# Optimization experiments

Measured on AMD Instinct MI355X. Metric: run time of the kernel, lower is better.

The kernel has to match this reference:

```python
import jax, jax.numpy as jnp
import numpy as np

Q, G, H, K, C, O = 20000, 20000, 32, 15, 128, 128


def setup_inputs() -> dict:
    key = jax.random.key(0)
    k1, k2, k3, k4, k5, k6 = jax.random.split(key, 6)
    return {
        "query_points": jax.random.normal(k1, (Q, 3), dtype=jnp.float32),
        "support_points": jax.random.normal(k2, (G, 3), dtype=jnp.float32),
        "support_features": jax.random.normal(k3, (G, C), dtype=jnp.float32),
        "kernel": jax.random.normal(k4, (K, 3), dtype=jnp.float32),
        "weights": jax.random.normal(k5, (K, C, O), dtype=jnp.float32),
        # KDTree KNN indices are precomputed int constants; random in-range
        # indices give identical math/perf characteristics.
        "neighbor_indices": jax.random.randint(k6, (Q, H), 0, G, dtype=jnp.int32),
    }


def reference(query_points, support_points, support_features, kernel, weights, neighbor_indices):
    # Faithful to original: neighbor_points gathered from query_points
    # (original code indexes query_points, not support_points; requires Q == G).
    neighbor_points = query_points[neighbor_indices]          # [Q, H, 3]
    neighbor_features = support_features[neighbor_indices]    # [Q, H, C]
    # diff: [Q, H, K, 3] = neighbor - query - kernel_point
    diff = neighbor_points[:, :, None, :] - query_points[:, None, None, :] - kernel
    distances = jnp.sqrt(jnp.sum(diff * diff, axis=-1))        # [Q, H, K]
    sigma = 1.0
    influences = jax.nn.relu(1.0 - distances / sigma)          # [Q, H, K]
    # 3-way contraction over h, k, c  -> [Q, O]
    result = jnp.einsum("qhk,kco,qhc->qo", influences, weights, neighbor_features)
    return result
```

## Files before the change

### kernel.cpp

```cpp
#include <hip/hip_runtime.h>


typedef short bf16x8 __attribute__((ext_vector_type(8)));
typedef float f32x4 __attribute__((ext_vector_type(4)));

constexpr int Qn = 20000;
constexpr int Hn = 32;
constexpr int Kn = 15;
constexpr int Cn = 128;
constexpr int On = 128;
constexpr int QB = 16;
constexpr int CK = 2048;
constexpr int KT = CK / 32;
constexpr int NT = On / 16;
constexpr int BLOCK = 512;

constexpr int F_OFF     = 0;
constexpr int NPT_OFF   = 0;
constexpr int DENSE_OFF = 8192;
constexpr int INFL_OFF  = 65536;
constexpr int GLIST_OFF = 81920;
constexpr int NIDX_OFF  = 83968;
constexpr int HLIST_OFF = 86016;
constexpr int CNT_OFF   = 87040;
constexpr int QPL_OFF   = 87104;
constexpr int KPL_OFF   = 87360;
constexpr int FLG_OFF   = 87616;
constexpr int POOL_SZ   = 87680;

__device__ __forceinline__ unsigned short f2bf(float x) {
  unsigned u = __float_as_uint(x);
  unsigned r = u + 0x7fffu + ((u >> 16) & 1u);
  return (unsigned short)(r >> 16);
}

__global__ void conv_w(const float* __restrict__ wts, unsigned short* __restrict__ wfrag) {
  int tid = blockIdx.x * 256 + threadIdx.x;
  if (tid >= KT * NT * 64) return;
  int l = tid & 63, nt = (tid >> 6) & 7, kt = tid >> 9;
  int col = nt * 16 + (l & 15);
  int ck0 = kt * 32 + (l >> 4) * 8;
  unsigned short v[8];
#pragma unroll
  for (int j = 0; j < 8; ++j) {
    int ck = ck0 + j;
    int k = ck & 15, c = ck >> 4;
    v[j] = (k < Kn) ? f2bf(wts[(k * Cn + c) * On + col]) : (unsigned short)0;
  }
  uint4 o;
  o.x = (unsigned)v[0] | ((unsigned)v[1] << 16);
  o.y = (unsigned)v[2] | ((unsigned)v[3] << 16);
  o.z = (unsigned)v[4] | ((unsigned)v[5] << 16);
  o.w = (unsigned)v[6] | ((unsigned)v[7] << 16);
  *(uint4*)(wfrag + (size_t)tid * 8) = o;
}

__global__ __launch_bounds__(BLOCK, 1)
void kpconv_main(const float* __restrict__ qpts,
                 const float* __restrict__ sfeat,
                 const float* __restrict__ kpts,
                 const int* __restrict__ nidx,
                 const unsigned short* __restrict__ wfrag,
                 float* __restrict__ out) {
  __shared__ __align__(16) char pool[POOL_SZ];
  const int t = threadIdx.x;
  const int qbase = blockIdx.x * QB;
  const int l = t & 63, w = t >> 6;
  const int lg = l >> 4, li = l & 15;

  {
    int g = nidx[(size_t)qbase * Hn + t];
    *(int*)(pool + NIDX_OFF + t * 4) = g;
    float* np = (float*)(pool + NPT_OFF + t * 16);
    np[0] = qpts[g * 3 + 0];
    np[1] = qpts[g * 3 + 1];
    np[2] = qpts[g * 3 + 2];
    uint4 z = {0, 0, 0, 0};
    *(uint4*)(pool + INFL_OFF + t * 32) = z;
    *(uint4*)(pool + INFL_OFF + t * 32 + 16) = z;
    if (t < 16) {
      *(unsigned*)(pool + FLG_OFF + t * 4) = 0u;
      float* qp = (float*)(pool + QPL_OFF + t * 16);
      qp[0] = qpts[(qbase + t) * 3 + 0];
      qp[1] = qpts[(qbase + t) * 3 + 1];
      qp[2] = qpts[(qbase + t) * 3 + 2];
    }
    if (t >= 32 && t < 32 + Kn) {
      int k = t - 32;
      float* kp = (float*)(pool + KPL_OFF + k * 16);
      kp[0] = kpts[k * 3 + 0];
      kp[1] = kpts[k * 3 + 1];
      kp[2] = kpts[k * 3 + 2];
    }
  }
  __syncthreads();

#pragma unroll
  for (int it = 0; it < 16; ++it) {
    int idx = t + it * BLOCK;
    int k = idx & 15, h = (idx >> 4) & 31, q = idx >> 9;
    unsigned short v = 0;
    if (k < Kn) {
      const float* np = (const float*)(pool + NPT_OFF + (q * 32 + h) * 16);
      const float* qp = (const float*)(pool + QPL_OFF + q * 16);
      const float* kp = (const float*)(pool + KPL_OFF + k * 16);
      float dx = np[0] - qp[0] - kp[0];
      float dy = np[1] - qp[1] - kp[1];
      float dz = np[2] - qp[2] - kp[2];
      float d = sqrtf(dx * dx + dy * dy + dz * dz);
      float inf = fmaxf(0.f, 1.f - d);
      if (inf > 0.f) atomicOr((unsigned*)(pool + FLG_OFF) + q, 1u << h);
      v = f2bf(inf);
    }
    *(unsigned short*)(pool + DENSE_OFF + q * 1024 + h * 32 + k * 2) = v;
  }
  __syncthreads();

  if (t < 16) {
    unsigned m = *(unsigned*)(pool + FLG_OFF + t * 4);
    int cnt = __popc(m);
    *(int*)(pool + CNT_OFF + t * 4) = cnt;
    int i = 0;
    while (m) {
      int h = __ffs(m) - 1; m &= m - 1;
      *(short*)(pool + HLIST_OFF + t * 64 + i * 2) = (short)h;
      *(int*)(pool + GLIST_OFF + t * 128 + i * 4) = *(int*)(pool + NIDX_OFF + (t * 32 + h) * 4);
      ++i;
    }
  }
  __syncthreads();

#pragma unroll
  for (int it = 0; it < 16; ++it) {
    int idx = t + it * BLOCK;
    int slot = idx & 31, k = (idx >> 5) & 15, q = idx >> 9;
    int cnt = *(const int*)(pool + CNT_OFF + q * 4);
    if (k < Kn && slot < cnt) {
      int h = *(const short*)(pool + HLIST_OFF + q * 64 + slot * 2);
      unsigned short v = *(const unsigned short*)(pool + DENSE_OFF + q * 1024 + h * 32 + k * 2);
      unsigned byte = (unsigned)(q * 1024) + (((unsigned)(k * 64 + slot * 2)) ^ (((unsigned)k & 7u) << 4));
      *(unsigned short*)(pool + INFL_OFF + byte) = v;
    }
  }
  __syncthreads();

  {
    const unsigned abase0 = (unsigned)INFL_OFF +
        (((unsigned)(li * 64 + lg * 16)) ^ (((unsigned)li & 7u) << 4));
    const int cbase = w * 16 + li;
    for (int q = 0; q < QB; ++q) {
      bf16x8 afrag = *(const bf16x8*)(pool + abase0 + q * 1024);
      uint4 ga = *(const uint4*)(pool + GLIST_OFF + q * 128 + lg * 32);
      uint4 gb = *(const uint4*)(pool + GLIST_OFF + q * 128 + lg * 32 + 16);
      int cnt = *(const int*)(pool + CNT_OFF + q * 4);
      int s0 = lg * 8;
      float v0 = (s0 + 0 < cnt) ? sfeat[(size_t)ga.x * Cn + cbase] : 0.f;
      float v1 = (s0 + 1 < cnt) ? sfeat[(size_t)ga.y * Cn + cbase] : 0.f;
      float v2 = (s0 + 2 < cnt) ? sfeat[(size_t)ga.z * Cn + cbase] : 0.f;
      float v3 = (s0 + 3 < cnt) ? sfeat[(size_t)ga.w * Cn + cbase] : 0.f;
      float v4 = (s0 + 4 < cnt) ? sfeat[(size_t)gb.x * Cn + cbase] : 0.f;
      float v5 = (s0 + 5 < cnt) ? sfeat[(size_t)gb.y * Cn + cbase] : 0.f;
      float v6 = (s0 + 6 < cnt) ? sfeat[(size_t)gb.z * Cn + cbase] : 0.f;
      float v7 = (s0 + 7 < cnt) ? sfeat[(size_t)gb.w * Cn + cbase] : 0.f;
      uint4 bu;
      bu.x = (unsigned)f2bf(v0) | ((unsigned)f2bf(v1) << 16);
      bu.y = (unsigned)f2bf(v2) | ((unsigned)f2bf(v3) << 16);
      bu.z = (unsigned)f2bf(v4) | ((unsigned)f2bf(v5) << 16);
      bu.w = (unsigned)f2bf(v6) | ((unsigned)f2bf(v7) << 16);
      bf16x8 bfrag = *(bf16x8*)&bu;
      f32x4 zero = {0.f, 0.f, 0.f, 0.f};
      f32x4 d = __builtin_amdgcn_mfma_f32_16x16x32_bf16(afrag, bfrag, zero, 0, 0, 0);
      unsigned wb = ((unsigned)(cbase * 32 + lg * 8) ^ (((unsigned)q & 7u) << 4)) + (unsigned)(q * 4096);
      uint2 pk;
      pk.x = (unsigned)f2bf(d[0]) | ((unsigned)f2bf(d[1]) << 16);
      pk.y = (unsigned)f2bf(d[2]) | ((unsigned)f2bf(d[3]) << 16);
      *(uint2*)(pool + F_OFF + wb) = pk;
    }
  }
  __syncthreads();

  {
    const int nt = w;
    const unsigned fb = (unsigned)(li * 4096 + lg * 16);
    const unsigned fswz = ((unsigned)li & 7u) << 4;
    const uint4* wf = (const uint4*)wfrag + (size_t)nt * 64 + l;
    f32x4 acc0 = {0.f, 0.f, 0.f, 0.f}, acc1 = {0.f, 0.f, 0.f, 0.f};
#pragma unroll 8
    for (int kt = 0; kt < KT; kt += 2) {
      bf16x8 a0 = *(const bf16x8*)(pool + F_OFF + ((fb + (unsigned)(kt * 64)) ^ fswz));
      uint4 w0 = wf[(size_t)kt * 512];
      bf16x8 a1 = *(const bf16x8*)(pool + F_OFF + ((fb + (unsigned)(kt * 64 + 64)) ^ fswz));
      uint4 w1 = wf[(size_t)kt * 512 + 512];
      acc0 = __builtin_amdgcn_mfma_f32_16x16x32_bf16(a0, *(bf16x8*)&w0, acc0, 0, 0, 0);
      acc1 = __builtin_amdgcn_mfma_f32_16x16x32_bf16(a1, *(bf16x8*)&w1, acc1, 0, 0, 0);
    }
    f32x4 acc = acc0 + acc1;
    float* obase = out + (size_t)qbase * On;
#pragma unroll
    for (int r = 0; r < 4; ++r)
      obase[(lg * 4 + r) * On + nt * 16 + li] = acc[r];
  }
}

extern "C" void kernel_launch(void* const* d_in, const int* in_sizes, int n_in,
                              void* d_out, int out_size, void* d_ws, size_t ws_size,
                              hipStream_t stream) {
  const float* qpts  = (const float*)d_in[0];
  const float* sfeat = (const float*)d_in[2];
  const float* kpts  = (const float*)d_in[3];
  const float* wts   = (const float*)d_in[4];
  const int*   nidx  = (const int*)d_in[5];
  float* outp = (float*)d_out;
  unsigned short* wfrag = (unsigned short*)d_ws;

  conv_w<<<(KT * NT * 64 + 255) / 256, 256, 0, stream>>>(wts, wfrag);
  kpconv_main<<<Qn / QB, BLOCK, 0, stream>>>(qpts, sfeat, kpts, nidx, wfrag, outp);
}
```

Baseline: 190.3 us.

## Split channel contraction into two LDS-halved passes to raise occupancy

```diff
diff --git a/kernel.cpp b/kernel.cpp
--- a/kernel.cpp
+++ b/kernel.cpp
@@ -1,4 +1,5 @@
 #include <hip/hip_runtime.h>
+#include <hip/hip_bf16.h>
 
 
 typedef short bf16x8 __attribute__((ext_vector_type(8)));
@@ -10,57 +11,53 @@
 constexpr int Cn = 128;
 constexpr int On = 128;
 constexpr int QB = 16;
-constexpr int CK = 2048;
-constexpr int KT = CK / 32;
-constexpr int NT = On / 16;
 constexpr int BLOCK = 512;
 
 constexpr int F_OFF     = 0;
 constexpr int NPT_OFF   = 0;
 constexpr int DENSE_OFF = 8192;
-constexpr int INFL_OFF  = 65536;
-constexpr int GLIST_OFF = 81920;
-constexpr int NIDX_OFF  = 83968;
-constexpr int HLIST_OFF = 86016;
-constexpr int CNT_OFF   = 87040;
-constexpr int QPL_OFF   = 87104;
-constexpr int KPL_OFF   = 87360;
-constexpr int FLG_OFF   = 87616;
-constexpr int POOL_SZ   = 87680;
-
-__device__ __forceinline__ unsigned short f2bf(float x) {
-  unsigned u = __float_as_uint(x);
-  unsigned r = u + 0x7fffu + ((u >> 16) & 1u);
-  return (unsigned short)(r >> 16);
-}
-
-__global__ void conv_w(const float* __restrict__ wts, unsigned short* __restrict__ wfrag) {
+constexpr int NIDX_OFF  = 24576;
+constexpr int HLIST_OFF = 26624;
+constexpr int QPL_OFF   = 27648;
+constexpr int KPL_OFF   = 27904;
+constexpr int FLG_OFF   = 28160;
+constexpr int INFL_OFF  = 32768;
+constexpr int GLIST_OFF = 49152;
+constexpr int CNT_OFF   = 51200;
+constexpr int POOL_SZ   = 51264;
+
+__device__ __forceinline__ unsigned short bfu(float x) {
+  union { __hip_bfloat16 h; unsigned short s; } cv;
+  cv.h = __float2bfloat16(x);
+  return cv.s;
+}
+__device__ __forceinline__ unsigned pk2(float a, float b) {
+  union { __hip_bfloat162 h2; unsigned u; } cv;
+  cv.h2 = __float22bfloat162_rn(make_float2(a, b));
+  return cv.u;
+}
+
+__global__ void conv_w(const float* __restrict__ wts, unsigned* __restrict__ wfrag) {
   int tid = blockIdx.x * 256 + threadIdx.x;
-  if (tid >= KT * NT * 64) return;
-  int l = tid & 63, nt = (tid >> 6) & 7, kt = tid >> 9;
-  int col = nt * 16 + (l & 15);
-  int ck0 = kt * 32 + (l >> 4) * 8;
-  unsigned short v[8];
-#pragma unroll
-  for (int j = 0; j < 8; ++j) {
-    int ck = ck0 + j;
-    int k = ck & 15, c = ck >> 4;
-    v[j] = (k < Kn) ? f2bf(wts[(k * Cn + c) * On + col]) : (unsigned short)0;
-  }
-  uint4 o;
-  o.x = (unsigned)v[0] | ((unsigned)v[1] << 16);
-  o.y = (unsigned)v[2] | ((unsigned)v[3] << 16);
-  o.z = (unsigned)v[4] | ((unsigned)v[5] << 16);
-  o.w = (unsigned)v[6] | ((unsigned)v[7] << 16);
-  *(uint4*)(wfrag + (size_t)tid * 8) = o;
-}
-
-__global__ __launch_bounds__(BLOCK, 1)
+  int wsel = tid & 3;
+  int l    = (tid >> 2) & 63;
+  int kt   = (tid >> 8) & 63;
+  int nt   = tid >> 14;
+  int col  = nt * 16 + (l & 15);
+  int ck   = kt * 32 + (l >> 4) * 8 + wsel * 2;
+  int k0 = ck & 15, c0 = ck >> 4;
+  int k1 = k0 + 1;
+  float a = wts[(k0 * Cn + c0) * On + col];
+  float b = (k1 < Kn) ? wts[(k1 * Cn + c0) * On + col] : 0.f;
+  wfrag[tid] = pk2(a, b);
+}
+
+__global__ __launch_bounds__(BLOCK, 4)
 void kpconv_main(const float* __restrict__ qpts,
                  const float* __restrict__ sfeat,
                  const float* __restrict__ kpts,
                  const int* __restrict__ nidx,
-                 const unsigned short* __restrict__ wfrag,
+                 const unsigned* __restrict__ wfrag,
                  float* __restrict__ out) {
   __shared__ __align__(16) char pool[POOL_SZ];
   const int t = threadIdx.x;
@@ -69,15 +66,13 @@
   const int lg = l >> 4, li = l & 15;
 
   {
+    *(unsigned*)(pool + GLIST_OFF + t * 4) = 0u;
     int g = nidx[(size_t)qbase * Hn + t];
     *(int*)(pool + NIDX_OFF + t * 4) = g;
     float* np = (float*)(pool + NPT_OFF + t * 16);
     np[0] = qpts[g * 3 + 0];
     np[1] = qpts[g * 3 + 1];
     np[2] = qpts[g * 3 + 2];
-    uint4 z = {0, 0, 0, 0};
-    *(uint4*)(pool + INFL_OFF + t * 32) = z;
-    *(uint4*)(pool + INFL_OFF + t * 32 + 16) = z;
     if (t < 16) {
       *(unsigned*)(pool + FLG_OFF + t * 4) = 0u;
       float* qp = (float*)(pool + QPL_OFF + t * 16);
@@ -110,7 +105,7 @@
       float d = sqrtf(dx * dx + dy * dy + dz * dz);
       float inf = fmaxf(0.f, 1.f - d);
       if (inf > 0.f) atomicOr((unsigned*)(pool + FLG_OFF) + q, 1u << h);
-      v = f2bf(inf);
+      v = bfu(inf);
     }
     *(unsigned short*)(pool + DENSE_OFF + q * 1024 + h * 32 + k * 2) = v;
   }
@@ -118,13 +113,13 @@
 
   if (t < 16) {
     unsigned m = *(unsigned*)(pool + FLG_OFF + t * 4);
-    int cnt = __popc(m);
-    *(int*)(pool + CNT_OFF + t * 4) = cnt;
+    *(int*)(pool + CNT_OFF + t * 4) = __popc(m);
     int i = 0;
     while (m) {
       int h = __ffs(m) - 1; m &= m - 1;
       *(short*)(pool + HLIST_OFF + t * 64 + i * 2) = (short)h;
-      *(int*)(pool + GLIST_OFF + t * 128 + i * 4) = *(int*)(pool + NIDX_OFF + (t * 32 + h) * 4);
+      *(int*)(pool + GLIST_OFF + t * 128 + i * 4) =
+          *(const int*)(pool + NIDX_OFF + (t * 32 + h) * 4);
       ++i;
     }
   }
@@ -135,24 +130,40 @@
     int idx = t + it * BLOCK;
     int slot = idx & 31, k = (idx >> 5) & 15, q = idx >> 9;
     int cnt = *(const int*)(pool + CNT_OFF + q * 4);
+    unsigned short v = 0;
     if (k < Kn && slot < cnt) {
       int h = *(const short*)(pool + HLIST_OFF + q * 64 + slot * 2);
-      unsigned short v = *(const unsigned short*)(pool + DENSE_OFF + q * 1024 + h * 32 + k * 2);
-      unsigned byte = (unsigned)(q * 1024) + (((unsigned)(k * 64 + slot * 2)) ^ (((unsigned)k & 7u) << 4));
-      *(unsigned short*)(pool + INFL_OFF + byte) = v;
-    }
-  }
-  __syncthreads();
-
-  {
-    const unsigned abase0 = (unsigned)INFL_OFF +
-        (((unsigned)(li * 64 + lg * 16)) ^ (((unsigned)li & 7u) << 4));
-    const int cbase = w * 16 + li;
-    for (int q = 0; q < QB; ++q) {
+      v = *(const unsigned short*)(pool + DENSE_OFF + q * 1024 + h * 32 + k * 2);
+    }
+    unsigned byte = (unsigned)(q * 1024) +
+        (((unsigned)(k * 64 + slot * 2)) ^ (((unsigned)k & 7u) << 4));
+    *(unsigned short*)(pool + INFL_OFF + byte) = v;
+  }
+  __syncthreads();
+
+  const int ctl = w & 3, qg = w >> 2;
+  const unsigned abase0 = (unsigned)INFL_OFF +
+      (((unsigned)(li * 64 + lg * 16)) ^ (((unsigned)li & 7u) << 4));
+  const int cl = ctl * 16 + li;
+  const unsigned wswz = ((unsigned)cl & 7u) << 4;
+  const unsigned wbase0 = (unsigned)((cl >> 1) * 1024 +
+                                     ((cl & 1) * 2 + (lg >> 1)) * 256 +
+                                     (lg & 1) * 8);
+  const unsigned liB = (unsigned)(lg * 256 + li * 16);
+  const unsigned sLg = ((unsigned)(lg >> 1)) << 4;
+  const uint4* wfp = (const uint4*)wfrag + (size_t)w * 4096 + l;
+  f32x4 acc0 = {0.f, 0.f, 0.f, 0.f}, acc1 = {0.f, 0.f, 0.f, 0.f};
+
+#pragma unroll 1
+  for (int r = 0; r < 2; ++r) {
+    const int cbase = r * 64 + cl;
+#pragma unroll 2
+    for (int qi = 0; qi < 8; ++qi) {
+      const int q = qg * 8 + qi;
+      int cnt = *(const int*)(pool + CNT_OFF + q * 4);
       bf16x8 afrag = *(const bf16x8*)(pool + abase0 + q * 1024);
       uint4 ga = *(const uint4*)(pool + GLIST_OFF + q * 128 + lg * 32);
       uint4 gb = *(const uint4*)(pool + GLIST_OFF + q * 128 + lg * 32 + 16);
-      int cnt = *(const int*)(pool + CNT_OFF + q * 4);
       int s0 = lg * 8;
       float v0 = (s0 + 0 < cnt) ? sfeat[(size_t)ga.x * Cn + cbase] : 0.f;
       float v1 = (s0 + 1 < cnt) ? sfeat[(size_t)ga.y * Cn + cbase] : 0.f;
@@ -163,42 +174,37 @@
       float v6 = (s0 + 6 < cnt) ? sfeat[(size_t)gb.z * Cn + cbase] : 0.f;
       float v7 = (s0 + 7 < cnt) ? sfeat[(size_t)gb.w * Cn + cbase] : 0.f;
       uint4 bu;
-      bu.x = (unsigned)f2bf(v0) | ((unsigned)f2bf(v1) << 16);
-      bu.y = (unsigned)f2bf(v2) | ((unsigned)f2bf(v3) << 16);
-      bu.z = (unsigned)f2bf(v4) | ((unsigned)f2bf(v5) << 16);
-      bu.w = (unsigned)f2bf(v6) | ((unsigned)f2bf(v7) << 16);
+      bu.x = pk2(v0, v1); bu.y = pk2(v2, v3);
+      bu.z = pk2(v4, v5); bu.w = pk2(v6, v7);
       bf16x8 bfrag = *(bf16x8*)&bu;
-      f32x4 zero = {0.f, 0.f, 0.f, 0.f};
-      f32x4 d = __builtin_amdgcn_mfma_f32_16x16x32_bf16(afrag, bfrag, zero, 0, 0, 0);
-      unsigned wb = ((unsigned)(cbase * 32 + lg * 8) ^ (((unsigned)q & 7u) << 4)) + (unsigned)(q * 4096);
-      uint2 pk;
-      pk.x = (unsigned)f2bf(d[0]) | ((unsigned)f2bf(d[1]) << 16);
-      pk.y = (unsigned)f2bf(d[2]) | ((unsigned)f2bf(d[3]) << 16);
-      *(uint2*)(pool + F_OFF + wb) = pk;
-    }
-  }
-  __syncthreads();
+      f32x4 z = {0.f, 0.f, 0.f, 0.f};
+      f32x4 d = __builtin_amdgcn_mfma_f32_16x16x32_bf16(afrag, bfrag, z, 0, 0, 0);
+      unsigned byte = (wbase0 + (unsigned)(q * 16)) ^ wswz;
+      *(uint2*)(pool + byte) = make_uint2(pk2(d[0], d[1]), pk2(d[2], d[3]));
+    }
+    __syncthreads();
+
+    const int ktbase = r * 32;
+#pragma unroll
+    for (int kt = 0; kt < 32; kt += 2) {
+      unsigned a0 = ((unsigned)(kt << 10) + liB) ^ (sLg | (((unsigned)kt & 3u) << 5));
+      unsigned a1 = ((unsigned)((kt + 1) << 10) + liB) ^ (sLg | (((unsigned)(kt + 1) & 3u) << 5));
+      bf16x8 f0 = *(const bf16x8*)(pool + a0);
+      uint4 w0 = wfp[(size_t)(ktbase + kt) * 64];
+      bf16x8 f1 = *(const bf16x8*)(pool + a1);
+      uint4 w1 = wfp[(size_t)(ktbase + kt + 1) * 64];
+      acc0 = __builtin_amdgcn_mfma_f32_16x16x32_bf16(f0, *(bf16x8*)&w0, acc0, 0, 0, 0);
+      acc1 = __builtin_amdgcn_mfma_f32_16x16x32_bf16(f1, *(bf16x8*)&w1, acc1, 0, 0, 0);
+    }
+    __syncthreads();
+  }
 
   {
-    const int nt = w;
-    const unsigned fb = (unsigned)(li * 4096 + lg * 16);
-    const unsigned fswz = ((unsigned)li & 7u) << 4;
-    const uint4* wf = (const uint4*)wfrag + (size_t)nt * 64 + l;
-    f32x4 acc0 = {0.f, 0.f, 0.f, 0.f}, acc1 = {0.f, 0.f, 0.f, 0.f};
-#pragma unroll 8
-    for (int kt = 0; kt < KT; kt += 2) {
-      bf16x8 a0 = *(const bf16x8*)(pool + F_OFF + ((fb + (unsigned)(kt * 64)) ^ fswz));
-      uint4 w0 = wf[(size_t)kt * 512];
-      bf16x8 a1 = *(const bf16x8*)(pool + F_OFF + ((fb + (unsigned)(kt * 64 + 64)) ^ fswz));
-      uint4 w1 = wf[(size_t)kt * 512 + 512];
-      acc0 = __builtin_amdgcn_mfma_f32_16x16x32_bf16(a0, *(bf16x8*)&w0, acc0, 0, 0, 0);
-      acc1 = __builtin_amdgcn_mfma_f32_16x16x32_bf16(a1, *(bf16x8*)&w1, acc1, 0, 0, 0);
-    }
     f32x4 acc = acc0 + acc1;
-    float* obase = out + (size_t)qbase * On;
-#pragma unroll
-    for (int r = 0; r < 4; ++r)
-      obase[(lg * 4 + r) * On + nt * 16 + li] = acc[r];
+    float* ob = out + (size_t)qbase * On + w * 16 + li;
+#pragma unroll
+    for (int rr = 0; rr < 4; ++rr)
+      ob[(lg * 4 + rr) * On] = acc[rr];
   }
 }
 
@@ -211,8 +217,8 @@
   const float* wts   = (const float*)d_in[4];
   const int*   nidx  = (const int*)d_in[5];
   float* outp = (float*)d_out;
-  unsigned short* wfrag = (unsigned short*)d_ws;
-
-  conv_w<<<(KT * NT * 64 + 255) / 256, 256, 0, stream>>>(wts, wfrag);
+  unsigned* wfrag = (unsigned*)d_ws;
+
+  conv_w<<<512, 256, 0, stream>>>(wts, wfrag);
   kpconv_main<<<Qn / QB, BLOCK, 0, stream>>>(qpts, sfeat, kpts, nidx, wfrag, outp);
 }
```

New measurement: 233.0 us. +22.4%, slower.
